# Kernel optimization log

Hardware: AMD Instinct MI355X
Metric: run time of the kernel (lower is better)

The kernel has to match this reference:

```python
import jax, jax.numpy as jnp
import numpy as np

NUM_HEADS = 4
EPS = 1e-12  # torch F.normalize eps


def conv1x1(x, w):
    # x: (b,c,h,w), w: (co,ci,1,1) -> pointwise conv == channel GEMM
    return jnp.einsum('bchw,dc->bdhw', x, w[:, :, 0, 0])


def dwconv3x3(x, w):
    # depthwise 3x3, groups = channels; w: (c,1,3,3)
    c = x.shape[1]
    return jax.lax.conv_general_dilated(
        x, w, window_strides=(1, 1), padding=((1, 1), (1, 1)),
        dimension_numbers=('NCHW', 'OIHW', 'NCHW'), feature_group_count=c)


def l2_normalize(x, axis=-1):
    n = jnp.sqrt(jnp.sum(x * x, axis=axis, keepdims=True))
    return x / jnp.maximum(n, EPS)


def setup_inputs() -> dict:
    key = jax.random.key(0)
    ks = jax.random.split(key, 8)
    b, c, h, w = 4, 192, 128, 128
    s = 0.05
    return {
        'x': jax.random.normal(ks[0], (b, c, h, w), jnp.float32),
        'wq': jax.random.normal(ks[1], (c, c, 1, 1), jnp.float32) * s,
        'wq_dw': jax.random.normal(ks[2], (c, 1, 3, 3), jnp.float32) * s,
        'wk': jax.random.normal(ks[3], (c, c, 1, 1), jnp.float32) * s,
        'wk_dw': jax.random.normal(ks[4], (c, 1, 3, 3), jnp.float32) * s,
        'wv': jax.random.normal(ks[5], (c, c, 1, 1), jnp.float32) * s,
        'wv_dw': jax.random.normal(ks[6], (c, 1, 3, 3), jnp.float32) * s,
        'temperature': jnp.ones((NUM_HEADS, 1, 1), jnp.float32),
    }


def reference(x, wq, wq_dw, wk, wk_dw, wv, wv_dw, temperature):
    b, c, h, w = x.shape
    hd = NUM_HEADS
    ch = c // hd  # per-head channels
    n = h * w

    q = dwconv3x3(conv1x1(x, wq), wq_dw)
    k = dwconv3x3(conv1x1(x, wk), wk_dw)
    v = dwconv3x3(conv1x1(x, wv), wv_dw)

    # b (head c) h w -> b head c (h w)
    q = q.reshape(b, hd, ch, n)
    k = k.reshape(b, hd, ch, n)
    v = v.reshape(b, hd, ch, n)

    q = l2_normalize(q, axis=-1)
    k = l2_normalize(k, axis=-1)

    # channel-wise attention: (c x N) @ (N x c) -> (c x c)
    attn = jnp.einsum('bhcn,bhdn->bhcd', q, k) * temperature  # temperature: (head,1,1)
    attn = jax.nn.softmax(attn, axis=-1)
    out = jnp.einsum('bhcd,bhdn->bhcn', attn, v)
    return out.reshape(b, c, h, w)
```

## Files before the change

### kernel.cpp

```cpp
#include <hip/hip_runtime.h>
#include <hip/hip_bf16.h>


typedef __attribute__((ext_vector_type(8))) short short8;
typedef __attribute__((ext_vector_type(4))) float f32x4;

#define NB 4
#define NC 192
#define NN 16384
#define CH 48
#define NWELEM 115780
#define NZERO 38400
#define LDP 200
#define AST 272
#define NCHUNK 32

__device__ inline unsigned short f2bf(float f) {
  union { float f; unsigned int u; } c; c.f = f;
  unsigned int r = c.u + 0x7FFF + ((c.u >> 16) & 1);
  return (unsigned short)(r >> 16);
}
__device__ inline float bf2f(unsigned short u) {
  union { unsigned int u; float f; } c; c.u = ((unsigned int)u) << 16;
  return c.f;
}

__device__ inline bool detect_f32(const unsigned short* x) {
  int l = threadIdx.x & 63;
  unsigned short u = x[2 * (l * 997 + 1)];
  int e = (u >> 7) & 0xFF;
  bool extreme = (e < 90) || (e > 165);
  return __popcll(__ballot(extreme)) >= 8;
}

__global__ __launch_bounds__(256) void k_pre(const unsigned short* __restrict__ x,
                                             const void* wq, const void* wk, const void* wv,
                                             const void* wqd, const void* wkd, const void* wvd,
                                             const void* temp,
                                             unsigned short* __restrict__ canon,
                                             float* __restrict__ zbase) {
  int blk = blockIdx.x;
  if (blk >= 453) {
    int i = (blk - 453) * 256 + threadIdx.x;
    if (i < NZERO) zbase[i] = 0.f;
    return;
  }
  bool f32 = detect_f32(x);
  int i = blk * 256 + threadIdx.x;
  if (i >= NWELEM) return;
  const void* src; int off;
  if (i < 36864)       { src = wq;  off = i; }
  else if (i < 73728)  { src = wk;  off = i - 36864; }
  else if (i < 110592) { src = wv;  off = i - 73728; }
  else if (i < 112320) { src = wqd; off = i - 110592; }
  else if (i < 114048) { src = wkd; off = i - 112320; }
  else if (i < 115776) { src = wvd; off = i - 114048; }
  else                 { src = temp; off = i - 115776; }
  canon[i] = f32 ? f2bf(((const float*)src)[off])
                 : ((const unsigned short*)src)[off];
}

__global__ __launch_bounds__(256) void k_conv(const unsigned short* __restrict__ Wall,
                                              const unsigned short* __restrict__ X,
                                              unsigned short* __restrict__ Yall) {
  __shared__ __align__(16) unsigned short Xs[128 * LDP];
  bool f32 = detect_f32(X);
  int b = blockIdx.y, p0 = blockIdx.x * 128;
  int tid = threadIdx.x;
  if (f32) {
    const float* Xf = (const float*)X + (size_t)b * NC * NN + p0;
    for (int it = 0; it < 12; ++it) {
      int idx = it * 256 + tid;
      int c = (idx >> 5) * 2, pq = idx & 31;
      float4 v0 = *(const float4*)(Xf + (size_t)c * NN + pq * 4);
      float4 v1 = *(const float4*)(Xf + (size_t)(c + 1) * NN + pq * 4);
#pragma unroll
      for (int j = 0; j < 4; ++j) {
        unsigned int u = ((unsigned int)f2bf((&v1.x)[j]) << 16) | f2bf((&v0.x)[j]);
        *(unsigned int*)(&Xs[(pq * 4 + j) * LDP + c]) = u;
      }
    }
  } else {
    const unsigned short* Xb = X + (size_t)b * NC * NN + p0;
    for (int it = 0; it < 12; ++it) {
      int idx = it * 256 + tid;
      int c = (idx >> 5) * 2, pq = idx & 31;
      ushort4 v0 = *(const ushort4*)(Xb + (size_t)c * NN + pq * 4);
      ushort4 v1 = *(const ushort4*)(Xb + (size_t)(c + 1) * NN + pq * 4);
#pragma unroll
      for (int j = 0; j < 4; ++j) {
        unsigned int u = ((unsigned int)((&v1.x)[j]) << 16) | (unsigned int)((&v0.x)[j]);
        *(unsigned int*)(&Xs[(pq * 4 + j) * LDP + c]) = u;
      }
    }
  }
  __syncthreads();
  int lane = tid & 63, w = tid >> 6;
  int wm = w & 1, wn = w >> 1;
  int lrow = lane & 15, lq = lane >> 4;
  short8 bf[6][4];
#pragma unroll
  for (int ks = 0; ks < 6; ++ks)
    for (int nt = 0; nt < 4; ++nt)
      bf[ks][nt] = *(const short8*)(&Xs[(wn * 64 + nt * 16 + lrow) * LDP + ks * 32 + lq * 8]);
  for (int dt = 0; dt < 9; ++dt) {
    int d0 = dt * 64;
    f32x4 acc[2][4];
    for (int mt = 0; mt < 2; ++mt)
      for (int nt = 0; nt < 4; ++nt) acc[mt][nt] = (f32x4){0.f, 0.f, 0.f, 0.f};
    for (int ks = 0; ks < 6; ++ks) {
      int k = ks * 32 + lq * 8;
      short8 a[2];
      for (int mt = 0; mt < 2; ++mt)
        a[mt] = *(const short8*)(Wall + (size_t)(d0 + wm * 32 + mt * 16 + lrow) * NC + k);
      for (int mt = 0; mt < 2; ++mt)
        for (int nt = 0; nt < 4; ++nt)
          acc[mt][nt] = __builtin_amdgcn_mfma_f32_16x16x32_bf16(a[mt], bf[ks][nt], acc[mt][nt], 0, 0, 0);
    }
    int proj = dt / 3, c0 = (dt % 3) * 64;
    unsigned short* Yb = Yall + (((size_t)proj * NB + b) * NC) * NN;
    for (int mt = 0; mt < 2; ++mt)
      for (int nt = 0; nt < 4; ++nt)
        for (int r = 0; r < 4; ++r) {
          int c = c0 + wm * 32 + mt * 16 + lq * 4 + r;
          int p = p0 + wn * 64 + nt * 16 + lrow;
          Yb[(size_t)c * NN + p] = f2bf(acc[mt][nt][r]);
        }
  }
}

__device__ inline void cvtrow(short8 raw, unsigned short lo, unsigned short hi,
                              float* dst) {
  dst[0] = bf2f(lo);
#pragma unroll
  for (int j = 0; j < 8; ++j) dst[j + 1] = bf2f((unsigned short)raw[j]);
  dst[9] = bf2f(hi);
}

__global__ __launch_bounds__(256) void k_dwconv(const unsigned short* __restrict__ Yall,
                                                const unsigned short* __restrict__ Wdall,
                                                unsigned short* __restrict__ Pq,
                                                unsigned short* __restrict__ Pk,
                                                unsigned short* __restrict__ Pv,
                                                float* __restrict__ ssq,
                                                float* __restrict__ ssk) {
  int y = blockIdx.x, b = blockIdx.y;
  int proj = y / NC, c = y % NC;
  int tid = threadIdx.x;
  int lane = tid & 63, ch = tid & 15, rg = tid >> 4;
  const unsigned short* base = Yall + (((size_t)proj * NB + b) * NC + c) * NN;
  unsigned short* P = (proj == 0 ? Pq : (proj == 1 ? Pk : Pv));
  float* ss = (proj == 0 ? ssq : (proj == 1 ? ssk : nullptr));
  int r0 = rg * 8;

  short8 raw[10];
  unsigned short hl[10], hr[10];
#pragma unroll
  for (int i = 0; i < 10; ++i) {
    int gy = r0 - 1 + i;
    const unsigned short* rp = base + gy * 128 + ch * 8;
    if (gy >= 0 && gy < 128) {
      raw[i] = *(const short8*)rp;
      hl[i] = (ch > 0)  ? rp[-1] : (unsigned short)0;
      hr[i] = (ch < 15) ? rp[8]  : (unsigned short)0;
    } else {
      raw[i] = (short8){0, 0, 0, 0, 0, 0, 0, 0};
      hl[i] = 0;
      hr[i] = 0;
    }
  }

  float wk9[9];
#pragma unroll
  for (int i = 0; i < 9; ++i) wk9[i] = bf2f(Wdall[(proj * NC + c) * 9 + i]);

  float rows[3][10];
  cvtrow(raw[0], hl[0], hr[0], rows[0]);
  cvtrow(raw[1], hl[1], hr[1], rows[1]);
  float ssacc = 0.f;
#pragma unroll
  for (int r = 0; r < 8; ++r) {
    cvtrow(raw[r + 2], hl[r + 2], hr[r + 2], rows[(r + 2) % 3]);
    float z[8];
#pragma unroll
    for (int j = 0; j < 8; ++j) z[j] = 0.f;
#pragma unroll
    for (int dy = 0; dy < 3; ++dy) {
      const float* f = rows[(r + dy) % 3];
      float w0 = wk9[dy * 3], w1 = wk9[dy * 3 + 1], w2 = wk9[dy * 3 + 2];
#pragma unroll
      for (int j = 0; j < 8; ++j) z[j] += w0 * f[j] + w1 * f[j + 1] + w2 * f[j + 2];
    }
    short8 sv;
#pragma unroll
    for (int j = 0; j < 8; ++j) { sv[j] = (short)f2bf(z[j]); ssacc += z[j] * z[j]; }
    *(short8*)(P + ((size_t)b * NC + c) * NN + (r0 + r) * 128 + ch * 8) = sv;
  }
  if (ss) {
    for (int off = 32; off; off >>= 1) ssacc += __shfl_down(ssacc, off);
    if (lane == 0) atomicAdd(&ss[b * NC + c], ssacc);
  }
}

__global__ __launch_bounds__(256) void k_attn(const unsigned short* __restrict__ Qp,
                                              const unsigned short* __restrict__ Kp,
                                              float* __restrict__ Spart) {
  __shared__ __align__(16) unsigned short Qs[CH * AST];
  __shared__ __align__(16) unsigned short Ks[CH * AST];
  __shared__ float Sred[CH * CH];
  int bh = blockIdx.y, chunk = blockIdx.x;
  int b = bh >> 2, h = bh & 3;
  int tid = threadIdx.x, lane = tid & 63, w = tid >> 6;
  int lrow = lane & 15, lq = lane >> 4;
  const unsigned short* Qb = Qp + ((size_t)b * NC + h * CH) * NN;
  const unsigned short* Kb = Kp + ((size_t)b * NC + h * CH) * NN;
  for (int i = tid; i < CH * CH; i += 256) Sred[i] = 0.f;
  f32x4 acc[3][3];
  for (int i = 0; i < 3; ++i)
    for (int j = 0; j < 3; ++j) acc[i][j] = (f32x4){0.f, 0.f, 0.f, 0.f};
#pragma unroll
  for (int rnd = 0; rnd < 2; ++rnd) {
    int n0 = chunk * 512 + rnd * 256;
    if (rnd) __syncthreads();
    for (int it = 0; it < 6; ++it) {
      int idx = it * 256 + tid;
      int row = idx >> 5, colv = idx & 31;
      *(short8*)(&Qs[row * AST + colv * 8]) = *(const short8*)(Qb + (size_t)row * NN + n0 + colv * 8);
      *(short8*)(&Ks[row * AST + colv * 8]) = *(const short8*)(Kb + (size_t)row * NN + n0 + colv * 8);
    }
    __syncthreads();
#pragma unroll
    for (int ks2 = 0; ks2 < 2; ++ks2) {
      int nn = (w * 2 + ks2) * 32 + lq * 8;
      short8 a[3], bb[3];
      for (int t = 0; t < 3; ++t) a[t]  = *(const short8*)(&Qs[(t * 16 + lrow) * AST + nn]);
      for (int t = 0; t < 3; ++t) bb[t] = *(const short8*)(&Ks[(t * 16 + lrow) * AST + nn]);
      for (int ti = 0; ti < 3; ++ti)
        for (int tj = 0; tj < 3; ++tj)
          acc[ti][tj] = __builtin_amdgcn_mfma_f32_16x16x32_bf16(a[ti], bb[tj], acc[ti][tj], 0, 0, 0);
    }
  }
  for (int ti = 0; ti < 3; ++ti)
    for (int tj = 0; tj < 3; ++tj)
      for (int r = 0; r < 4; ++r) {
        int row = ti * 16 + lq * 4 + r, col = tj * 16 + lrow;
        atomicAdd(&Sred[row * CH + col], acc[ti][tj][r]);
      }
  __syncthreads();
  float* Sg = Spart + ((size_t)chunk * 16 + bh) * (CH * CH);
  for (int i = tid; i < CH * CH; i += 256) Sg[i] = Sred[i];
}

__global__ __launch_bounds__(256) void k_reduce(const float* __restrict__ Spart,
                                                float* __restrict__ S) {
  int bh = blockIdx.y;
  int e = blockIdx.x * 256 + threadIdx.x;
  const float* P = Spart + (size_t)bh * (CH * CH) + e;
  float s = 0.f;
#pragma unroll 8
  for (int c = 0; c < NCHUNK; ++c) s += P[(size_t)c * 16 * (CH * CH)];
  S[(size_t)bh * (CH * CH) + e] = s;
}

__global__ void k_softmax(const float* __restrict__ S, const float* __restrict__ ssq,
                          const float* __restrict__ ssk, const unsigned short* __restrict__ tempc,
                          float* __restrict__ AT) {
  int bh = blockIdx.x, b = bh >> 2, h = bh & 3;
  int i = threadIdx.x;
  if (i >= CH) return;
  float t = bf2f(tempc[h]);
  float rq = 1.f / fmaxf(sqrtf(ssq[b * NC + h * CH + i]), 1e-12f);
  const float* Srow = S + bh * (CH * CH) + i * CH;
  float l[CH];
  float m = -1e30f;
  for (int j = 0; j < CH; ++j) {
    float rk = 1.f / fmaxf(sqrtf(ssk[b * NC + h * CH + j]), 1e-12f);
    l[j] = Srow[j] * rq * rk * t;
    m = fmaxf(m, l[j]);
  }
  float s = 0.f;
  for (int j = 0; j < CH; ++j) { l[j] = __expf(l[j] - m); s += l[j]; }
  float inv = 1.f / s;
  for (int j = 0; j < CH; ++j) AT[bh * (CH * CH) + j * CH + i] = l[j] * inv;
}

__global__ __launch_bounds__(256) void k_out(const float* __restrict__ AT,
                                             const unsigned short* __restrict__ Vp,
                                             void* __restrict__ Out,
                                             const unsigned short* __restrict__ x) {
  __shared__ float As[CH * CH];
  bool f32 = detect_f32(x);
  int bh = blockIdx.y, b = bh >> 2, h = bh & 3;
  int tid = threadIdx.x;
  int pxs = tid & 63, islot = tid >> 6;
  int p0 = blockIdx.x * 256 + pxs * 4;
  int i0 = islot * 12;
  const float* A = AT + bh * (CH * CH);
  for (int it = 0; it < 9; ++it) As[it * 256 + tid] = A[it * 256 + tid];
  __syncthreads();
  const unsigned short* Vb = Vp + ((size_t)b * NC + h * CH) * NN;
  float acc[12][4];
#pragma unroll
  for (int ii = 0; ii < 12; ++ii)
    for (int q = 0; q < 4; ++q) acc[ii][q] = 0.f;
  for (int j = 0; j < CH; ++j) {
    ushort4 vv = *(const ushort4*)(Vb + (size_t)j * NN + p0);
    float v0 = bf2f(vv.x), v1 = bf2f(vv.y), v2 = bf2f(vv.z), v3 = bf2f(vv.w);
    const float* Aj = As + j * CH + i0;
#pragma unroll
    for (int ii = 0; ii < 12; ++ii) {
      float a = Aj[ii];
      acc[ii][0] += a * v0;
      acc[ii][1] += a * v1;
      acc[ii][2] += a * v2;
      acc[ii][3] += a * v3;
    }
  }
  size_t obase = ((size_t)b * NC + h * CH) * NN;
  if (f32) {
    float* Of = (float*)Out;
#pragma unroll
    for (int ii = 0; ii < 12; ++ii) {
      float4 o = make_float4(acc[ii][0], acc[ii][1], acc[ii][2], acc[ii][3]);
      *(float4*)(Of + obase + (size_t)(i0 + ii) * NN + p0) = o;
    }
  } else {
    unsigned short* Ob = (unsigned short*)Out;
#pragma unroll
    for (int ii = 0; ii < 12; ++ii) {
      ushort4 sv;
      sv.x = f2bf(acc[ii][0]); sv.y = f2bf(acc[ii][1]);
      sv.z = f2bf(acc[ii][2]); sv.w = f2bf(acc[ii][3]);
      *(ushort4*)(Ob + obase + (size_t)(i0 + ii) * NN + p0) = sv;
    }
  }
}

extern "C" void kernel_launch(void* const* d_in, const int* in_sizes, int n_in,
                              void* d_out, int out_size, void* d_ws, size_t ws_size,
                              hipStream_t stream) {
  const unsigned short* x = (const unsigned short*)d_in[0];

  const size_t TEN = (size_t)NB * NC * NN;
  unsigned short* bufA = (unsigned short*)d_ws;
  unsigned short* bufB = bufA + TEN;
  unsigned short* bufV = bufB + TEN;
  unsigned short* Yall = bufV + TEN;
  float* ssq = (float*)(Yall + 3 * TEN);
  float* ssk = ssq + NB * NC;
  float* S   = ssk + NB * NC;
  float* AT  = S + 16 * CH * CH;
  unsigned short* canon = (unsigned short*)(AT + 16 * CH * CH);
  float* Spart = (float*)(canon + 115782);
  const unsigned short* Wall = canon;
  const unsigned short* Wdall = canon + 110592;
  const unsigned short* Tmp = canon + 115776;

  k_pre<<<453 + (NZERO + 255) / 256, 256, 0, stream>>>(
      x, d_in[1], d_in[3], d_in[5], d_in[2], d_in[4], d_in[6], d_in[7], canon, ssq);
  k_conv<<<dim3(NN / 128, NB), 256, 0, stream>>>(Wall, x, Yall);
  k_dwconv<<<dim3(3 * NC, NB), 256, 0, stream>>>(Yall, Wdall, bufA, bufB, bufV, ssq, ssk);
  k_attn<<<dim3(NCHUNK, 16), 256, 0, stream>>>(bufA, bufB, Spart);
  k_reduce<<<dim3(9, 16), 256, 0, stream>>>(Spart, S);
  k_softmax<<<16, 64, 0, stream>>>(S, ssq, ssk, Tmp, AT);
  k_out<<<dim3(NN / 256, 16), 256, 0, stream>>>(AT, bufV, d_out, x);
}
```

Before: 237.7 us.

## Fuse partial-sum reduction into softmax, change conv input load pattern, shrink zeroing

Merges the k_reduce kernel into k_softmax so the chunk partial sums are reduced into shared memory inside the softmax block, removing one launch and the global round trip through S. The k_conv input staging now uses scalar per-pixel loads with a different thread mapping instead of float4 loads, which changes coalescing and the LDS write pattern. NZERO is shrunk, so the pre-kernel zeroes much less memory. The fused softmax runs only 16 blocks for the reduction, which limits parallelism, and the scalar loads may lower load efficiency.

```diff
diff --git a/kernel.cpp b/kernel.cpp
--- a/kernel.cpp
+++ b/kernel.cpp
@@ -10,7 +10,7 @@
 #define NN 16384
 #define CH 48
 #define NWELEM 115780
-#define NZERO 38400
+#define NZERO 1536
 #define LDP 200
 #define AST 272
 #define NCHUNK 32
@@ -67,30 +67,31 @@
   bool f32 = detect_f32(X);
   int b = blockIdx.y, p0 = blockIdx.x * 128;
   int tid = threadIdx.x;
+  int tq = tid & 15, cq = tid >> 4;
   if (f32) {
     const float* Xf = (const float*)X + (size_t)b * NC * NN + p0;
-    for (int it = 0; it < 12; ++it) {
-      int idx = it * 256 + tid;
-      int c = (idx >> 5) * 2, pq = idx & 31;
-      float4 v0 = *(const float4*)(Xf + (size_t)c * NN + pq * 4);
-      float4 v1 = *(const float4*)(Xf + (size_t)(c + 1) * NN + pq * 4);
-#pragma unroll
-      for (int j = 0; j < 4; ++j) {
-        unsigned int u = ((unsigned int)f2bf((&v1.x)[j]) << 16) | f2bf((&v0.x)[j]);
-        *(unsigned int*)(&Xs[(pq * 4 + j) * LDP + c]) = u;
+    for (int outer = 0; outer < 6; ++outer) {
+      int c = (cq + outer * 16) * 2;
+      const float* r0p = Xf + (size_t)c * NN;
+      const float* r1p = Xf + (size_t)(c + 1) * NN;
+#pragma unroll
+      for (int jp = 0; jp < 8; ++jp) {
+        int px = tq + jp * 16;
+        unsigned int u = ((unsigned int)f2bf(r1p[px]) << 16) | f2bf(r0p[px]);
+        *(unsigned int*)(&Xs[px * LDP + c]) = u;
       }
     }
   } else {
     const unsigned short* Xb = X + (size_t)b * NC * NN + p0;
-    for (int it = 0; it < 12; ++it) {
-      int idx = it * 256 + tid;
-      int c = (idx >> 5) * 2, pq = idx & 31;
-      ushort4 v0 = *(const ushort4*)(Xb + (size_t)c * NN + pq * 4);
-      ushort4 v1 = *(const ushort4*)(Xb + (size_t)(c + 1) * NN + pq * 4);
-#pragma unroll
-      for (int j = 0; j < 4; ++j) {
-        unsigned int u = ((unsigned int)((&v1.x)[j]) << 16) | (unsigned int)((&v0.x)[j]);
-        *(unsigned int*)(&Xs[(pq * 4 + j) * LDP + c]) = u;
+    for (int outer = 0; outer < 6; ++outer) {
+      int c = (cq + outer * 16) * 2;
+      const unsigned short* r0p = Xb + (size_t)c * NN;
+      const unsigned short* r1p = Xb + (size_t)(c + 1) * NN;
+#pragma unroll
+      for (int jp = 0; jp < 8; ++jp) {
+        int px = tq + jp * 16;
+        unsigned int u = ((unsigned int)r1p[px] << 16) | (unsigned int)r0p[px];
+        *(unsigned int*)(&Xs[px * LDP + c]) = u;
       }
     }
   }
@@ -251,31 +252,32 @@
   for (int i = tid; i < CH * CH; i += 256) Sg[i] = Sred[i];
 }
 
-__global__ __launch_bounds__(256) void k_reduce(const float* __restrict__ Spart,
-                                                float* __restrict__ S) {
-  int bh = blockIdx.y;
-  int e = blockIdx.x * 256 + threadIdx.x;
-  const float* P = Spart + (size_t)bh * (CH * CH) + e;
-  float s = 0.f;
+__global__ __launch_bounds__(256) void k_softmax(const float* __restrict__ Spart,
+                                                 const float* __restrict__ ssq,
+                                                 const float* __restrict__ ssk,
+                                                 const unsigned short* __restrict__ tempc,
+                                                 float* __restrict__ AT) {
+  __shared__ float Ssum[CH * CH];
+  int bh = blockIdx.x, b = bh >> 2, h = bh & 3;
+  int tid = threadIdx.x;
+  for (int it = 0; it < 9; ++it) {
+    int e = it * 256 + tid;
+    const float* P = Spart + (size_t)bh * (CH * CH) + e;
+    float s = 0.f;
 #pragma unroll 8
-  for (int c = 0; c < NCHUNK; ++c) s += P[(size_t)c * 16 * (CH * CH)];
-  S[(size_t)bh * (CH * CH) + e] = s;
-}
-
-__global__ void k_softmax(const float* __restrict__ S, const float* __restrict__ ssq,
-                          const float* __restrict__ ssk, const unsigned short* __restrict__ tempc,
-                          float* __restrict__ AT) {
-  int bh = blockIdx.x, b = bh >> 2, h = bh & 3;
-  int i = threadIdx.x;
+    for (int c = 0; c < NCHUNK; ++c) s += P[(size_t)c * 16 * (CH * CH)];
+    Ssum[e] = s;
+  }
+  __syncthreads();
+  int i = tid;
   if (i >= CH) return;
   float t = bf2f(tempc[h]);
   float rq = 1.f / fmaxf(sqrtf(ssq[b * NC + h * CH + i]), 1e-12f);
-  const float* Srow = S + bh * (CH * CH) + i * CH;
   float l[CH];
   float m = -1e30f;
   for (int j = 0; j < CH; ++j) {
     float rk = 1.f / fmaxf(sqrtf(ssk[b * NC + h * CH + j]), 1e-12f);
-    l[j] = Srow[j] * rq * rk * t;
+    l[j] = Ssum[i * CH + j] * rq * rk * t;
     m = fmaxf(m, l[j]);
   }
   float s = 0.f;
@@ -361,7 +363,6 @@
   k_conv<<<dim3(NN / 128, NB), 256, 0, stream>>>(Wall, x, Yall);
   k_dwconv<<<dim3(3 * NC, NB), 256, 0, stream>>>(Yall, Wdall, bufA, bufB, bufV, ssq, ssk);
   k_attn<<<dim3(NCHUNK, 16), 256, 0, stream>>>(bufA, bufB, Spart);
-  k_reduce<<<dim3(9, 16), 256, 0, stream>>>(Spart, S);
-  k_softmax<<<16, 64, 0, stream>>>(S, ssq, ssk, Tmp, AT);
+  k_softmax<<<16, 256, 0, stream>>>(Spart, ssq, ssk, Tmp, AT);
   k_out<<<dim3(NN / 256, 16), 256, 0, stream>>>(AT, bufV, d_out, x);
 }
```

After: 250.7 us. 5.5% more time.
